# Kernel optimization log

Hardware: AMD Instinct MI355X
Metric: run time of the kernel (lower is better)

The kernel has to match this reference:

```python
import jax, jax.numpy as jnp
import numpy as np

TEMPERATURE = 0.07
EPS = 1e-8  # torch CosineSimilarity eps


def setup_inputs() -> dict:
    key = jax.random.key(0)
    features = jax.random.normal(key, (16, 1024, 512), dtype=jnp.float32)
    return {"features": features}


def reference(features):
    """Vectorized equivalent of the original double Python loop.

    For each b and each t in [1, T-2]:
      anchor = f[b,t], positive = f[b,t+1]
      negatives = all frames j with j < t-1 or j >= t+2  (excludes t-1, t, t+1)
      loss_bt = -log( exp(cos(a,p)/T) / (exp(cos(a,p)/T) + sum_j exp(cos(a,n_j)/T)) )
    Returns mean over all (b, t) pairs (neg pool is non-empty for all t when T > 3).
    """
    B, T, D = features.shape
    norm = jnp.maximum(jnp.linalg.norm(features, axis=-1, keepdims=True), EPS)
    n = features / norm  # [B, T, D]
    # full pairwise cosine-sim logits, scaled by temperature
    sim = jnp.einsum('btd,bsd->bts', n, n) / TEMPERATURE  # [B, T, T]

    t_idx = jnp.arange(1, T - 1)            # anchors t = 1 .. T-2
    j_idx = jnp.arange(T)
    # negatives: j in [0, t-1) union [t+2, T)  -> excludes t-1, t, t+1
    neg_mask = (j_idx[None, :] < t_idx[:, None] - 1) | (j_idx[None, :] >= t_idx[:, None] + 2)  # [T-2, T]

    logits = sim[:, 1:T - 1, :]                                   # [B, T-2, T]
    pos = logits[:, jnp.arange(T - 2), jnp.arange(2, T)]          # sim[b, t, t+1] -> [B, T-2]
    neg_logits = jnp.where(neg_mask[None], logits, -jnp.inf)
    lse_neg = jax.nn.logsumexp(neg_logits, axis=-1)               # log sum_j exp(neg_sim)
    # -log(exp(pos)/(exp(pos)+negsum)) = logaddexp(pos, lse_neg) - pos
    loss_bt = jnp.logaddexp(pos, lse_neg) - pos                   # [B, T-2]
    return jnp.mean(loss_bt)
```

## Files before the change

kernel.cpp:

```cpp
#include <hip/hip_runtime.h>
#include <hip/hip_bf16.h>

#define B_ 16
#define T_ 1024
#define D_ 512
#define INV_TEMP 14.285714285714286f
#define EPS_ 1e-8f

#define BM 128
#define BN 128
#define BKK 32
#define NKIT (D_ / BKK)

typedef __attribute__((ext_vector_type(8))) short short8;
typedef __attribute__((ext_vector_type(4))) float floatx4;

typedef __attribute__((address_space(1))) const unsigned int g_u32;
typedef __attribute__((address_space(3))) unsigned int l_u32;

__device__ __forceinline__ void glds16(const void* g, void* l) {
    __builtin_amdgcn_global_load_lds((g_u32*)g, (l_u32*)l, 16, 0, 0);
}

__device__ __forceinline__ unsigned short f2bf(float x) {
    unsigned u = __float_as_uint(x);
    return (unsigned short)((u + 0x7fffu + ((u >> 16) & 1u)) >> 16);
}

__global__ void zero_kernel(float* __restrict__ rs_g, float* __restrict__ rp_g,
                            float* __restrict__ out) {
    const int i = blockIdx.x * 256 + threadIdx.x;
    if (i < B_ * T_) { rs_g[i] = 0.0f; rp_g[i] = 0.0f; }
    if (i == 0) out[0] = 0.0f;
}

__global__ __launch_bounds__(256) void norm_kernel(const float* __restrict__ f,
                                                   unsigned short* __restrict__ nrm) {
    const int row  = blockIdx.x * 4 + (threadIdx.x >> 6);
    const int lane = threadIdx.x & 63;
    const size_t off = (size_t)row * D_ + lane * 8;
    const float4 v0 = *(const float4*)(f + off);
    const float4 v1 = *(const float4*)(f + off + 4);
    float ss = v0.x*v0.x + v0.y*v0.y + v0.z*v0.z + v0.w*v0.w
             + v1.x*v1.x + v1.y*v1.y + v1.z*v1.z + v1.w*v1.w;
    #pragma unroll
    for (int o = 32; o >= 1; o >>= 1) ss += __shfl_xor(ss, o, 64);
    const float sc = 1.0f / fmaxf(sqrtf(ss), EPS_);
    ushort4 w0, w1;
    w0.x = f2bf(v0.x*sc); w0.y = f2bf(v0.y*sc); w0.z = f2bf(v0.z*sc); w0.w = f2bf(v0.w*sc);
    w1.x = f2bf(v1.x*sc); w1.y = f2bf(v1.y*sc); w1.z = f2bf(v1.z*sc); w1.w = f2bf(v1.w*sc);
    *(ushort4*)(nrm + off)     = w0;
    *(ushort4*)(nrm + off + 4) = w1;
}

__global__ __launch_bounds__(256) void loss_kernel(const unsigned short* __restrict__ nrm,
                                                   float* __restrict__ rs_g,
                                                   float* __restrict__ rp_g) {
    const int b  = blockIdx.y;
    const int t0 = blockIdx.x * BM;
    const int j0 = blockIdx.z * BN;
    const char* base = (const char*)(nrm + (size_t)b * T_ * D_);

    __shared__ __align__(16) unsigned short As[BM * BKK];
    __shared__ __align__(16) unsigned short Bs[BN * BKK];

    const int tid  = threadIdx.x;
    const int w    = tid >> 6;
    const int lane = tid & 63;
    const int wr   = w >> 1;
    const int wc   = w & 1;
    const int m    = lane & 15;
    const int kq   = lane >> 4;

    const int o0 = (w * 2 + 0) * 1024 + lane * 16;
    const int o1 = (w * 2 + 1) * 1024 + lane * 16;
    const char* gA0 = base + (size_t)(t0 + (o0 >> 6)) * 1024 + (o0 & 63);
    const char* gA1 = base + (size_t)(t0 + (o1 >> 6)) * 1024 + (o1 & 63);
    const char* gB0 = base + (size_t)(j0 + (o0 >> 6)) * 1024 + (o0 & 63);
    const char* gB1 = base + (size_t)(j0 + (o1 >> 6)) * 1024 + (o1 & 63);
    char* lA0 = (char*)As + (w * 2 + 0) * 1024;
    char* lA1 = (char*)As + (w * 2 + 1) * 1024;
    char* lB0 = (char*)Bs + (w * 2 + 0) * 1024;
    char* lB1 = (char*)Bs + (w * 2 + 1) * 1024;

    floatx4 acc[4][4] = {};

    for (int kit = 0; kit < NKIT; ++kit) {
        const int kb = kit * 64;
        glds16(gA0 + kb, lA0);
        glds16(gA1 + kb, lA1);
        glds16(gB0 + kb, lB0);
        glds16(gB1 + kb, lB1);
        __syncthreads();

        short8 a[4], bf[4];
        #pragma unroll
        for (int mi = 0; mi < 4; ++mi)
            a[mi] = *(const short8*)(As + (wr * 64 + mi * 16 + m) * BKK + kq * 8);
        #pragma unroll
        for (int ni = 0; ni < 4; ++ni)
            bf[ni] = *(const short8*)(Bs + (wc * 64 + ni * 16 + m) * BKK + kq * 8);

        #pragma unroll
        for (int mi = 0; mi < 4; ++mi)
            #pragma unroll
            for (int ni = 0; ni < 4; ++ni)
                acc[mi][ni] = __builtin_amdgcn_mfma_f32_16x16x32_bf16(
                    a[mi], bf[ni], acc[mi][ni], 0, 0, 0);

        __syncthreads();
    }

    const int lrow = lane >> 4;
    const int lcol = lane & 15;
    #pragma unroll
    for (int mi = 0; mi < 4; ++mi) {
        #pragma unroll
        for (int r = 0; r < 4; ++r) {
            const int t = t0 + wr * 64 + mi * 16 + lrow * 4 + r;
            float rs = 0.0f, rp = 0.0f;
            #pragma unroll
            for (int ni = 0; ni < 4; ++ni) {
                const int j = j0 + wc * 64 + ni * 16 + lcol;
                const float s = acc[mi][ni][r] * INV_TEMP;
                const float e = __expf(s);
                if (j < t - 1 || j > t + 1) rs += e;
                if (j == t + 1)             rp  = s;
            }
            #pragma unroll
            for (int o = 8; o >= 1; o >>= 1) {
                rs += __shfl_xor(rs, o, 64);
                rp += __shfl_xor(rp, o, 64);
            }
            if (lcol == 0) {
                atomicAdd(&rs_g[b * T_ + t], rs);
                atomicAdd(&rp_g[b * T_ + t], rp);
            }
        }
    }
}

__global__ __launch_bounds__(256) void fin_kernel(const float* __restrict__ rs_g,
                                                  const float* __restrict__ rp_g,
                                                  float* __restrict__ out) {
    const int idx = blockIdx.x * 256 + threadIdx.x;
    float v = 0.0f;
    if (idx < B_ * T_) {
        const int t = idx & (T_ - 1);
        if (t >= 1 && t <= T_ - 2) {
            const float pos  = rp_g[idx];
            const float sneg = rs_g[idx];
            v = logf(__expf(pos) + sneg) - pos;
        }
    }
    #pragma unroll
    for (int o = 32; o >= 1; o >>= 1) v += __shfl_xor(v, o, 64);
    __shared__ float ws_[4];
    if ((threadIdx.x & 63) == 0) ws_[threadIdx.x >> 6] = v;
    __syncthreads();
    if (threadIdx.x == 0) {
        const float scale = 1.0f / (float)(B_ * (T_ - 2));
        atomicAdd(out, (ws_[0] + ws_[1] + ws_[2] + ws_[3]) * scale);
    }
}

extern "C" void kernel_launch(void* const* d_in, const int* in_sizes, int n_in,
                              void* d_out, int out_size, void* d_ws, size_t ws_size,
                              hipStream_t stream) {
    const float* feat = (const float*)d_in[0];
    float* out = (float*)d_out;

    unsigned short* nrm = (unsigned short*)d_ws;
    float* rs_g = (float*)((char*)d_ws + (size_t)B_ * T_ * D_ * sizeof(unsigned short));
    float* rp_g = rs_g + B_ * T_;

    zero_kernel<<<(B_ * T_ + 255) / 256, 256, 0, stream>>>(rs_g, rp_g, out);
    norm_kernel<<<B_ * T_ / 4, 256, 0, stream>>>(feat, nrm);
    loss_kernel<<<dim3(T_ / BM, B_, T_ / BN), 256, 0, stream>>>(nrm, rs_g, rp_g);
    fin_kernel<<<(B_ * T_ + 255) / 256, 256, 0, stream>>>(rs_g, rp_g, out);
}
```

Before: 114.4 us.

## Exploit similarity symmetry, load MFMA fragments directly from global, fuse zeroing into norm

```diff
diff --git a/kernel.cpp b/kernel.cpp
--- a/kernel.cpp
+++ b/kernel.cpp
@@ -4,38 +4,32 @@
 #define B_ 16
 #define T_ 1024
 #define D_ 512
-#define INV_TEMP 14.285714285714286f
 #define EPS_ 1e-8f
+#define SCALE2 20.609929155566063f
+#define LN2_ 0.6931471805599453f
 
 #define BM 128
 #define BN 128
-#define BKK 32
-#define NKIT (D_ / BKK)
+#define NB 8
+#define NKIT 16
 
 typedef __attribute__((ext_vector_type(8))) short short8;
 typedef __attribute__((ext_vector_type(4))) float floatx4;
-
-typedef __attribute__((address_space(1))) const unsigned int g_u32;
-typedef __attribute__((address_space(3))) unsigned int l_u32;
-
-__device__ __forceinline__ void glds16(const void* g, void* l) {
-    __builtin_amdgcn_global_load_lds((g_u32*)g, (l_u32*)l, 16, 0, 0);
-}
 
 __device__ __forceinline__ unsigned short f2bf(float x) {
     unsigned u = __float_as_uint(x);
     return (unsigned short)((u + 0x7fffu + ((u >> 16) & 1u)) >> 16);
 }
 
-__global__ void zero_kernel(float* __restrict__ rs_g, float* __restrict__ rp_g,
-                            float* __restrict__ out) {
-    const int i = blockIdx.x * 256 + threadIdx.x;
-    if (i < B_ * T_) { rs_g[i] = 0.0f; rp_g[i] = 0.0f; }
-    if (i == 0) out[0] = 0.0f;
-}
+__global__ __launch_bounds__(256) void norm_kernel(const float* __restrict__ f,
+                                                   unsigned short* __restrict__ nrm,
+                                                   float* __restrict__ rs_g,
+                                                   float* __restrict__ rp_g,
+                                                   float* __restrict__ out) {
+    const int gi = blockIdx.x * 256 + threadIdx.x;
+    if (gi < B_ * T_) { rs_g[gi] = 0.0f; rp_g[gi] = 0.0f; }
+    if (gi == 0) out[0] = 0.0f;
 
-__global__ __launch_bounds__(256) void norm_kernel(const float* __restrict__ f,
-                                                   unsigned short* __restrict__ nrm) {
     const int row  = blockIdx.x * 4 + (threadIdx.x >> 6);
     const int lane = threadIdx.x & 63;
     const size_t off = (size_t)row * D_ + lane * 8;
@@ -56,13 +50,15 @@
 __global__ __launch_bounds__(256) void loss_kernel(const unsigned short* __restrict__ nrm,
                                                    float* __restrict__ rs_g,
                                                    float* __restrict__ rp_g) {
+    int u = blockIdx.x, bi = 0, rem = NB;
+    while (u >= rem) { u -= rem; --rem; ++bi; }
+    const int bj   = bi + u;
+    const bool diag = (bi == bj);
+
     const int b  = blockIdx.y;
-    const int t0 = blockIdx.x * BM;
-    const int j0 = blockIdx.z * BN;
-    const char* base = (const char*)(nrm + (size_t)b * T_ * D_);
-
-    __shared__ __align__(16) unsigned short As[BM * BKK];
-    __shared__ __align__(16) unsigned short Bs[BN * BKK];
+    const int t0 = bi * BM;
+    const int j0 = bj * BN;
+    const unsigned short* base = nrm + (size_t)b * T_ * D_;
 
     const int tid  = threadIdx.x;
     const int w    = tid >> 6;
@@ -72,70 +68,72 @@
     const int m    = lane & 15;
     const int kq   = lane >> 4;
 
-    const int o0 = (w * 2 + 0) * 1024 + lane * 16;
-    const int o1 = (w * 2 + 1) * 1024 + lane * 16;
-    const char* gA0 = base + (size_t)(t0 + (o0 >> 6)) * 1024 + (o0 & 63);
-    const char* gA1 = base + (size_t)(t0 + (o1 >> 6)) * 1024 + (o1 & 63);
-    const char* gB0 = base + (size_t)(j0 + (o0 >> 6)) * 1024 + (o0 & 63);
-    const char* gB1 = base + (size_t)(j0 + (o1 >> 6)) * 1024 + (o1 & 63);
-    char* lA0 = (char*)As + (w * 2 + 0) * 1024;
-    char* lA1 = (char*)As + (w * 2 + 1) * 1024;
-    char* lB0 = (char*)Bs + (w * 2 + 0) * 1024;
-    char* lB1 = (char*)Bs + (w * 2 + 1) * 1024;
+    const unsigned short* pA[4];
+    const unsigned short* pB[4];
+    #pragma unroll
+    for (int i = 0; i < 4; ++i) {
+        pA[i] = base + (size_t)(t0 + wr * 64 + i * 16 + m) * D_ + kq * 8;
+        pB[i] = base + (size_t)(j0 + wc * 64 + i * 16 + m) * D_ + kq * 8;
+    }
 
     floatx4 acc[4][4] = {};
+    short8 af[2][4], bf[2][4];
+    #pragma unroll
+    for (int i = 0; i < 4; ++i) {
+        af[0][i] = *(const short8*)(pA[i]);
+        bf[0][i] = *(const short8*)(pB[i]);
+    }
 
+    #pragma unroll
     for (int kit = 0; kit < NKIT; ++kit) {
-        const int kb = kit * 64;
-        glds16(gA0 + kb, lA0);
-        glds16(gA1 + kb, lA1);
-        glds16(gB0 + kb, lB0);
-        glds16(gB1 + kb, lB1);
-        __syncthreads();
-
-        short8 a[4], bf[4];
-        #pragma unroll
-        for (int mi = 0; mi < 4; ++mi)
-            a[mi] = *(const short8*)(As + (wr * 64 + mi * 16 + m) * BKK + kq * 8);
-        #pragma unroll
-        for (int ni = 0; ni < 4; ++ni)
-            bf[ni] = *(const short8*)(Bs + (wc * 64 + ni * 16 + m) * BKK + kq * 8);
-
+        const int cur = kit & 1, nxt = cur ^ 1;
+        if (kit + 1 < NKIT) {
+            #pragma unroll
+            for (int i = 0; i < 4; ++i) {
+                af[nxt][i] = *(const short8*)(pA[i] + (kit + 1) * 32);
+                bf[nxt][i] = *(const short8*)(pB[i] + (kit + 1) * 32);
+            }
+        }
         #pragma unroll
         for (int mi = 0; mi < 4; ++mi)
             #pragma unroll
             for (int ni = 0; ni < 4; ++ni)
                 acc[mi][ni] = __builtin_amdgcn_mfma_f32_16x16x32_bf16(
-                    a[mi], bf[ni], acc[mi][ni], 0, 0, 0);
-
-        __syncthreads();
+                    af[cur][mi], bf[cur][ni], acc[mi][ni], 0, 0, 0);
     }
 
     const int lrow = lane >> 4;
     const int lcol = lane & 15;
+    const int bT   = b * T_;
+    float cs[4] = {0.f, 0.f, 0.f, 0.f};
+
     #pragma unroll
     for (int mi = 0; mi < 4; ++mi) {
         #pragma unroll
         for (int r = 0; r < 4; ++r) {
             const int t = t0 + wr * 64 + mi * 16 + lrow * 4 + r;
-            float rs = 0.0f, rp = 0.0f;
+            float rsum = 0.f;
             #pragma unroll
             for (int ni = 0; ni < 4; ++ni) {
-                const int j = j0 + wc * 64 + ni * 16 + lcol;
-                const float s = acc[mi][ni][r] * INV_TEMP;
-                const float e = __expf(s);
-                if (j < t - 1 || j > t + 1) rs += e;
-                if (j == t + 1)             rp  = s;
+                const int j  = j0 + wc * 64 + ni * 16 + lcol;
+                const float s2 = acc[mi][ni][r] * SCALE2;
+                const float e  = exp2f(s2);
+                if (j < t - 1 || j > t + 1) { rsum += e; cs[ni] += e; }
+                if (j == t + 1) atomicAdd(&rp_g[bT + t], s2);
             }
             #pragma unroll
-            for (int o = 8; o >= 1; o >>= 1) {
-                rs += __shfl_xor(rs, o, 64);
-                rp += __shfl_xor(rp, o, 64);
-            }
-            if (lcol == 0) {
-                atomicAdd(&rs_g[b * T_ + t], rs);
-                atomicAdd(&rp_g[b * T_ + t], rp);
-            }
+            for (int o = 8; o >= 1; o >>= 1) rsum += __shfl_xor(rsum, o, 64);
+            if (lcol == 0) atomicAdd(&rs_g[bT + t], rsum);
+        }
+    }
+    if (!diag) {
+        #pragma unroll
+        for (int ni = 0; ni < 4; ++ni) {
+            float c = cs[ni];
+            c += __shfl_xor(c, 16, 64);
+            c += __shfl_xor(c, 32, 64);
+            if (lrow == 0)
+                atomicAdd(&rs_g[bT + j0 + wc * 64 + ni * 16 + lcol], c);
         }
     }
 }
@@ -148,9 +146,9 @@
     if (idx < B_ * T_) {
         const int t = idx & (T_ - 1);
         if (t >= 1 && t <= T_ - 2) {
-            const float pos  = rp_g[idx];
-            const float sneg = rs_g[idx];
-            v = logf(__expf(pos) + sneg) - pos;
+            const float p2 = rp_g[idx];
+            const float s  = rs_g[idx];
+            v = (log2f(exp2f(p2) + s) - p2) * LN2_;
         }
     }
     #pragma unroll
@@ -174,8 +172,7 @@
     float* rs_g = (float*)((char*)d_ws + (size_t)B_ * T_ * D_ * sizeof(unsigned short));
     float* rp_g = rs_g + B_ * T_;
 
-    zero_kernel<<<(B_ * T_ + 255) / 256, 256, 0, stream>>>(rs_g, rp_g, out);
-    norm_kernel<<<B_ * T_ / 4, 256, 0, stream>>>(feat, nrm);
-    loss_kernel<<<dim3(T_ / BM, B_, T_ / BN), 256, 0, stream>>>(nrm, rs_g, rp_g);
+    norm_kernel<<<B_ * T_ / 4, 256, 0, stream>>>(feat, nrm, rs_g, rp_g, out);
+    loss_kernel<<<dim3(NB * (NB + 1) / 2, B_), 256, 0, stream>>>(nrm, rs_g, rp_g);
     fin_kernel<<<(B_ * T_ + 255) / 256, 256, 0, stream>>>(rs_g, rp_g, out);
 }
```

After: 147.6 us. 29.0% more time.
